# Optimization experiments

Hardware: AMD Instinct MI355X
Metric: run time of the kernel (lower is better)

The kernel has to match this reference:

```python
import jax, jax.numpy as jnp
import numpy as np

N_NODES = 200000
N_EDGES = 6400000
IN_CH, HID, OUT_CH = 14, 16, 2


def gcn_conv(x, W, b, src, dst, n_nodes):
    """GCNConv with self-loops and symmetric normalization (PyG defaults).

    out[i] = sum_{j->i} d[i]^-1/2 d[j]^-1/2 (xW)[j] + d[i]^-1 (xW)[i] + b,
    where d = degree(A + I) computed on the target index.
    """
    h = x @ W  # [N, F_out]
    ones = jnp.ones((src.shape[0],), dtype=x.dtype)
    deg = jax.ops.segment_sum(ones, dst, num_segments=n_nodes) + 1.0  # +1 self-loop
    dinv = jax.lax.rsqrt(deg)  # [N]
    norm = dinv[src] * dinv[dst]  # [E]
    msg = h[src] * norm[:, None]  # [E, F_out] -- dominant memory traffic
    agg = jax.ops.segment_sum(msg, dst, num_segments=n_nodes)
    self_loop = h * (dinv * dinv)[:, None]
    return agg + self_loop + b


def setup_inputs() -> dict:
    key = jax.random.key(0)
    k1, k2, k3, k4, k5 = jax.random.split(key, 5)
    x = jax.random.normal(k1, (N_NODES, IN_CH), dtype=jnp.float32)
    edge_index = jax.random.randint(k2, (2, N_EDGES), 0, N_NODES, dtype=jnp.int64)
    edge_attr = jax.random.normal(k3, (N_EDGES, 1), dtype=jnp.float32)  # unused by GCNConv
    s = 1.0 / np.sqrt(IN_CH)
    W1 = jax.random.uniform(k4, (IN_CH, HID), jnp.float32, -s, s)
    b1 = jnp.zeros((HID,), jnp.float32)
    s2 = 1.0 / np.sqrt(HID)
    W2 = jax.random.uniform(k5, (HID, OUT_CH), jnp.float32, -s2, s2)
    b2 = jnp.zeros((OUT_CH,), jnp.float32)
    return {"x": x, "edge_index": edge_index, "edge_attr": edge_attr,
            "W1": W1, "b1": b1, "W2": W2, "b2": b2}


def reference(x, edge_index, edge_attr, W1, b1, W2, b2):
    src, dst = edge_index[0], edge_index[1]
    n = x.shape[0]
    h = jax.nn.relu(gcn_conv(x, W1, b1, src, dst, n))
    # F.dropout(training=self.training) is identity in eval mode
    out = gcn_conv(h, W2, b2, src, dst, n)
    return out
```

## Files before the change

kernel.cpp:

```cpp
#include <hip/hip_runtime.h>
#include <hip/hip_fp16.h>


constexpr int NN = 200000;
constexpr int NE = 6400000;
constexpr int IC = 14;
constexpr int HC = 16;
constexpr int OC = 2;

constexpr int NBK = 392;
constexpr int NSUB = 8;
constexpr int SCAP = 2816;
constexpr int NSEG = NSUB * NBK;
constexpr int CCAP = NSUB * SCAP;
constexpr int SPT = (SCAP + 1023) / 1024;
constexpr int TILE = 5120;
constexpr int BTH = 512;
constexpr int IPT = TILE / BTH;
constexpr int IPT2 = IPT / 2;
constexpr int NTILE = NE / TILE;
constexpr int OVFCAP = 65536;
constexpr int NM = NN / 32;
constexpr int GSTR = 16;

typedef unsigned long long ull;
typedef float f4v __attribute__((ext_vector_type(4)));

__device__ __forceinline__ int phase_of(unsigned src) {
    return src >= 100000u ? (src >= 150000u ? 3 : 2) : (src >= 50000u ? 1 : 0);
}

__device__ __forceinline__ int xcc_id() {
    int x;
    asm volatile("s_getreg_b32 %0, hwreg(HW_REG_XCC_ID)" : "=s"(x));
    return x & 7;
}

__global__ void k_init(int* __restrict__ gcur, const void* __restrict__ ei,
                       int* __restrict__ flag) {
    int i = blockIdx.x * blockDim.x + threadIdx.x;
    if (i < NSEG) gcur[i * GSTR] = i * SCAP;
    else if (i <= NSEG + 4) gcur[i * GSTR] = 0;
    if (i == 500) {
        const ull* p = (const ull*)ei;
        ull acc = 0ULL;
        for (int k = 0; k < 64; ++k) acc |= (p[k] >> 32);
        *flag = (acc == 0ULL) ? 1 : 0;
    }
}

__global__ __launch_bounds__(BTH, 6) void k_binA(const void* __restrict__ ei,
                                                 const int* __restrict__ flag,
                                                 int* __restrict__ gcur,
                                                 unsigned* __restrict__ binned,
                                                 ull* __restrict__ ovf) {
    __shared__ int hist[NBK];
    __shared__ int lofs[NBK];
    __shared__ int gofs[NBK];
    __shared__ int wsum[BTH / 64];
    __shared__ unsigned stage[TILE];

    int t = threadIdx.x;
    int fl = *flag;
    int tile0 = blockIdx.x * TILE;
    int segbase = xcc_id() * NBK;

    if (t < NBK) hist[t] = 0;
    __syncthreads();

    int dbuf[IPT], sbuf[IPT];
    const int* pw = (const int*)ei;
    if (fl) {
#pragma unroll
        for (int k = 0; k < IPT2; ++k) {
            int e = tile0 + k * (2 * BTH) + 2 * t;
            dbuf[2 * k] = pw[2 * (NE + e)];
            dbuf[2 * k + 1] = pw[2 * (NE + e) + 2];
            sbuf[2 * k] = pw[2 * e];
            sbuf[2 * k + 1] = pw[2 * e + 2];
        }
    } else {
#pragma unroll
        for (int k = 0; k < IPT2; ++k) {
            int e = tile0 + k * (2 * BTH) + 2 * t;
            uint2 dd = *(const uint2*)(pw + NE + e);
            uint2 ss = *(const uint2*)(pw + e);
            dbuf[2 * k] = (int)dd.x;
            dbuf[2 * k + 1] = (int)dd.y;
            sbuf[2 * k] = (int)ss.x;
            sbuf[2 * k + 1] = (int)ss.y;
        }
    }

    unsigned pk[IPT];
    unsigned ra[IPT];
#pragma unroll
    for (int k = 0; k < IPT; ++k) {
        int d = dbuf[k];
        int b = d >> 9;
        int r = atomicAdd(&hist[b], 1);
        pk[k] = ((unsigned)(d & 511) << 18) | (unsigned)sbuf[k];
        ra[k] = ((unsigned)r << 9) | (unsigned)b;
    }
    __syncthreads();

    int h0 = 0, h1 = 0, p = 0;
    if (t < NBK / 2) {
        h0 = hist[2 * t];
        h1 = hist[2 * t + 1];
        p = h0 + h1;
    }
    int lane = t & 63;
    int w = t >> 6;
    int incl = p;
#pragma unroll
    for (int off = 1; off < 64; off <<= 1) {
        int v = __shfl_up(incl, off, 64);
        if (lane >= off) incl += v;
    }
    if (lane == 63) wsum[w] = incl;
    __syncthreads();
    int wbase = 0;
#pragma unroll
    for (int ww = 0; ww < BTH / 64; ++ww) wbase += (ww < w) ? wsum[ww] : 0;
    int ex = wbase + incl - p;
    if (t < NBK / 2) {
        lofs[2 * t] = ex;
        lofs[2 * t + 1] = ex + h0;
    }
    if (t < NBK) gofs[t] = atomicAdd(&gcur[(segbase + t) * GSTR], hist[t]);
    __syncthreads();

#pragma unroll
    for (int k = 0; k < IPT; ++k) {
        int b = (int)(ra[k] & 511u);
        int r = (int)(ra[k] >> 9);
        stage[lofs[b] + r] = pk[k];
    }
    __syncthreads();

    for (int i = t; i < TILE; i += BTH) {
        int b = (i * 313) >> 12;
        if (b > NBK - 1) b = NBK - 1;
        while (b < NBK - 1 && lofs[b + 1] <= i) ++b;
        while (lofs[b] > i) --b;
        unsigned pack = stage[i];
        int seg = segbase + b;
        int dest = gofs[b] + (i - lofs[b]);
        if (dest < (seg + 1) * SCAP) {
            binned[dest] = pack;
        } else {
            int op = atomicAdd(&gcur[NSEG * GSTR], 1);
            if (op < OVFCAP) {
                int d = (b << 9) | (int)(pack >> 18);
                int s = (int)(pack & 0x3FFFF);
                ovf[op] = ((ull)d << 32) | (unsigned)s;
            }
        }
    }
}

__global__ __launch_bounds__(1024, 4) void k_sort(const int* __restrict__ gcur,
                                                  const unsigned* __restrict__ binned,
                                                  const ull* __restrict__ ovf,
                                                  unsigned* __restrict__ csr,
                                                  float* __restrict__ dinv,
                                                  int* __restrict__ rsg,
                                                  unsigned* __restrict__ spl) {
    __shared__ int cnt[2048];
    __shared__ int excl[2048];
    __shared__ int wsum[16];
    __shared__ int nseg[NSUB];
    __shared__ unsigned stage[CCAP];
    int b = blockIdx.x;
    int t = threadIdx.x;
    cnt[t] = 0;
    cnt[t + 1024] = 0;
    if (t < NSUB) {
        int seg = t * NBK + b;
        nseg[t] = min(gcur[seg * GSTR] - seg * SCAP, SCAP);
    }
    __syncthreads();
    int nov = min(gcur[NSEG * GSTR], OVFCAP);

    unsigned srcv[NSUB * SPT];
    unsigned rkv[NSUB * SPT];
#pragma unroll
    for (int s = 0; s < NSUB; ++s) {
        int n = nseg[s];
        int sb = (s * NBK + b) * SCAP;
#pragma unroll
        for (int k = 0; k < SPT; ++k) {
            int i = k * 1024 + t;
            rkv[s * SPT + k] = 0xFFFFFFFFu;
            if (i < n) {
                unsigned pack = binned[sb + i];
                unsigned src = pack & 0x3FFFFu;
                int key = ((int)(pack >> 18) << 2) | phase_of(src);
                int r = atomicAdd(&cnt[key], 1);
                srcv[s * SPT + k] = src;
                rkv[s * SPT + k] = ((unsigned)r << 11) | (unsigned)key;
            }
        }
    }
    __syncthreads();

    int h0 = cnt[2 * t];
    int h1 = cnt[2 * t + 1];
    int p = h0 + h1;
    int lane = t & 63;
    int w = t >> 6;
    int incl = p;
#pragma unroll
    for (int off = 1; off < 64; off <<= 1) {
        int v = __shfl_up(incl, off, 64);
        if (lane >= off) incl += v;
    }
    if (lane == 63) wsum[w] = incl;
    __syncthreads();
    int wbase = 0;
#pragma unroll
    for (int ww = 0; ww < 16; ++ww) wbase += (ww < w) ? wsum[ww] : 0;
    int ex = wbase + incl - p;
    excl[2 * t] = ex;
    excl[2 * t + 1] = ex + h0;
    __syncthreads();

#pragma unroll
    for (int c = 0; c < NSUB * SPT; ++c) {
        unsigned rk = rkv[c];
        if (rk != 0xFFFFFFFFu) {
            int key = (int)(rk & 0x7FFu);
            int r = (int)(rk >> 11);
            stage[excl[key] + r] = srcv[c];
        }
    }

    if (t < 512) {
        int g = (b << 9) + t;
        if (g < NN) {
            int c0 = cnt[4 * t];
            int c1 = cnt[4 * t + 1];
            int c2 = cnt[4 * t + 2];
            int c3 = cnt[4 * t + 3];
            int extra = 0;
            for (int k = 0; k < nov; ++k) extra += ((int)(ovf[k] >> 32) == g);
            dinv[g] = rsqrtf((float)(c0 + c1 + c2 + c3 + extra) + 1.0f);
            rsg[g] = b * CCAP + excl[4 * t];
            spl[g] = (unsigned)c0 | ((unsigned)c1 << 8) |
                     ((unsigned)c2 << 16) | ((unsigned)c3 << 24);
        }
    }
    __syncthreads();

    int total = excl[2047] + cnt[2047];
    int tot4 = (total + 3) >> 2;
    const uint4* st4 = (const uint4*)stage;
    uint4* csr4 = (uint4*)(csr + (size_t)b * CCAP);
#pragma unroll
    for (int k = 0; k < (CCAP / 4 + 1023) / 1024; ++k) {
        int i4 = k * 1024 + t;
        if (i4 < tot4) csr4[i4] = st4[i4];
    }
}

__global__ void k_prep(const float* __restrict__ x, const float* __restrict__ dinv,
                       __half* __restrict__ xph) {
    int i = blockIdx.x * blockDim.x + threadIdx.x;
    if (i >= NN * 16) return;
    int node = i >> 4;
    int c = i & 15;
    float v = (c < IC) ? dinv[node] * x[node * IC + c] : 0.0f;
    xph[i] = __float2half(v);
}

__global__ __launch_bounds__(256) void k_agg1(const int* __restrict__ rsg,
                                              const unsigned* __restrict__ spl,
                                              const unsigned* __restrict__ csr,
                                              const __half* __restrict__ xph,
                                              float* __restrict__ partial) {
    int t = threadIdx.x;
    int q2 = blockIdx.x & 1;
    int blk = blockIdx.x >> 1;
    int g = t >> 3;
    int qq = t & 3;
    int eh = (t >> 2) & 1;
    int i = blk * 32 + g;
    unsigned sp = spl[i];
    int c0 = (int)(sp & 255u);
    int c1 = (int)((sp >> 8) & 255u);
    int beg = rsg[i] + (q2 ? c0 : 0);
    int end = beg + (q2 ? c1 : c0);

    float ax = 0.0f, ay = 0.0f, az = 0.0f, aw = 0.0f;
    int j = beg + eh;
    int s0 = (j < end) ? (int)csr[j] : -1;
    int s1 = (j + 2 < end) ? (int)csr[j + 2] : -1;
    while (j < end) {
        int jn = j + 4;
        int n0 = (jn < end) ? (int)csr[jn] : -1;
        int n1 = (jn + 2 < end) ? (int)csr[jn + 2] : -1;
        uint2 u0 = *(const uint2*)(xph + (size_t)s0 * 16 + 4 * qq);
        float2 f0 = __half22float2(*(__half2*)&u0.x);
        float2 f1 = __half22float2(*(__half2*)&u0.y);
        ax += f0.x;
        ay += f0.y;
        az += f1.x;
        aw += f1.y;
        if (s1 >= 0) {
            uint2 u1 = *(const uint2*)(xph + (size_t)s1 * 16 + 4 * qq);
            float2 f2 = __half22float2(*(__half2*)&u1.x);
            float2 f3 = __half22float2(*(__half2*)&u1.y);
            ax += f2.x;
            ay += f2.y;
            az += f3.x;
            aw += f3.y;
        }
        s0 = n0;
        s1 = n1;
        j = jn;
    }
    ax += __shfl_xor(ax, 4);
    ay += __shfl_xor(ay, 4);
    az += __shfl_xor(az, 4);
    aw += __shfl_xor(aw, 4);
    if (eh == 0) {
        f4v r = {ax, ay, az, aw};
        __builtin_nontemporal_store(
            r, (f4v*)(partial + ((size_t)q2 * NN + i) * 16 + 4 * qq));
    }
}

__global__ __launch_bounds__(256) void k_agg1m(const int* __restrict__ rsg,
                                               const unsigned* __restrict__ spl,
                                               const unsigned* __restrict__ csr,
                                               const __half* __restrict__ xph,
                                               const float* __restrict__ partial,
                                               const int* __restrict__ gcur,
                                               const ull* __restrict__ ovf,
                                               const float* __restrict__ dinv,
                                               const float* __restrict__ W1,
                                               const float* __restrict__ b1,
                                               const float* __restrict__ W2,
                                               const float* __restrict__ b2,
                                               float2* __restrict__ h2bp,
                                               float2* __restrict__ selfout) {
    __shared__ float sW1[IC * HC];
    __shared__ float sb1[HC];
    __shared__ float sW2[HC * OC];
    __shared__ float sb2[OC];
    __shared__ float sAgg[32][17];
    int t = threadIdx.x;
    if (t < IC * HC) sW1[t] = W1[t];
    if (t < HC) sb1[t] = b1[t];
    if (t < HC * OC) sW2[t] = W2[t];
    if (t < OC) sb2[t] = b2[t];

    int g = t >> 3;
    int qq = t & 3;
    int eh = (t >> 2) & 1;
    int i = blockIdx.x * 32 + g;
    unsigned sp = spl[i];
    int c0 = (int)(sp & 255u);
    int c1 = (int)((sp >> 8) & 255u);
    int c2 = (int)((sp >> 16) & 255u);
    int c3 = (int)(sp >> 24);
    int beg = rsg[i] + c0 + c1;
    int end = beg + c2 + c3;

    float ax = 0.0f, ay = 0.0f, az = 0.0f, aw = 0.0f;
    int j = beg + eh;
    int s0 = (j < end) ? (int)csr[j] : -1;
    int s1 = (j + 2 < end) ? (int)csr[j + 2] : -1;
    while (j < end) {
        int jn = j + 4;
        int n0 = (jn < end) ? (int)csr[jn] : -1;
        int n1 = (jn + 2 < end) ? (int)csr[jn + 2] : -1;
        uint2 u0 = *(const uint2*)(xph + (size_t)s0 * 16 + 4 * qq);
        float2 f0 = __half22float2(*(__half2*)&u0.x);
        float2 f1 = __half22float2(*(__half2*)&u0.y);
        ax += f0.x;
        ay += f0.y;
        az += f1.x;
        aw += f1.y;
        if (s1 >= 0) {
            uint2 u1 = *(const uint2*)(xph + (size_t)s1 * 16 + 4 * qq);
            float2 f2 = __half22float2(*(__half2*)&u1.x);
            float2 f3 = __half22float2(*(__half2*)&u1.y);
            ax += f2.x;
            ay += f2.y;
            az += f3.x;
            aw += f3.y;
        }
        s0 = n0;
        s1 = n1;
        j = jn;
    }

    if (eh == 0) {
        f4v a0 = __builtin_nontemporal_load(
            (const f4v*)(partial + (size_t)i * 16 + 4 * qq));
        uint2 us = *(const uint2*)(xph + (size_t)i * 16 + 4 * qq);
        float2 sx = __half22float2(*(__half2*)&us.x);
        float2 sy = __half22float2(*(__half2*)&us.y);
        ax += a0.x + sx.x;
        ay += a0.y + sx.y;
        az += a0.z + sy.x;
        aw += a0.w + sy.y;
    } else {
        f4v a1 = __builtin_nontemporal_load(
            (const f4v*)(partial + ((size_t)NN + i) * 16 + 4 * qq));
        ax += a1.x;
        ay += a1.y;
        az += a1.z;
        aw += a1.w;
    }
    ax += __shfl_xor(ax, 4);
    ay += __shfl_xor(ay, 4);
    az += __shfl_xor(az, 4);
    aw += __shfl_xor(aw, 4);

    float dv = dinv[i];
    if (eh == 0) {
        int nov = min(gcur[NSEG * GSTR], OVFCAP);
        for (int k = 0; k < nov; ++k) {
            ull e = ovf[k];
            if ((int)(e >> 32) == i) {
                int s = (int)(e & 0xFFFFFFFFu);
                int ch = 4 * qq;
                ax += __half2float(xph[(size_t)s * 16 + ch]);
                ay += __half2float(xph[(size_t)s * 16 + ch + 1]);
                az += __half2float(xph[(size_t)s * 16 + ch + 2]);
                aw += __half2float(xph[(size_t)s * 16 + ch + 3]);
            }
        }
        sAgg[g][4 * qq + 0] = dv * ax;
        sAgg[g][4 * qq + 1] = dv * ay;
        sAgg[g][4 * qq + 2] = dv * az;
        sAgg[g][4 * qq + 3] = dv * aw;
    }
    __syncthreads();

    int l8 = t & 7;
    float o0 = 0.0f, o1 = 0.0f;
#pragma unroll
    for (int f2 = 0; f2 < 2; ++f2) {
        int f = 2 * l8 + f2;
        float a = sb1[f];
#pragma unroll
        for (int c = 0; c < IC; ++c) a = fmaf(sAgg[g][c], sW1[c * HC + f], a);
        a = fmaxf(a, 0.0f);
        o0 = fmaf(a, sW2[f * OC + 0], o0);
        o1 = fmaf(a, sW2[f * OC + 1], o1);
    }
    o0 += __shfl_xor(o0, 1);
    o1 += __shfl_xor(o1, 1);
    o0 += __shfl_xor(o0, 2);
    o1 += __shfl_xor(o1, 2);
    o0 += __shfl_xor(o0, 4);
    o1 += __shfl_xor(o1, 4);
    if (l8 == 0) {
        h2bp[i] = make_float2(o0 * dv, o1 * dv);
        selfout[i] = make_float2(o0 * dv * dv + sb2[0], o1 * dv * dv + sb2[1]);
    }
}

__global__ __launch_bounds__(256) void k_agg2(const int* __restrict__ rsg,
                                              const unsigned* __restrict__ spl,
                                              const unsigned* __restrict__ csr,
                                              const int* __restrict__ gcur,
                                              const ull* __restrict__ ovf,
                                              const float* __restrict__ dinv,
                                              const float2* __restrict__ h2bp,
                                              const float2* __restrict__ selfout,
                                              float2* __restrict__ out) {
    int tt = blockIdx.x * 256 + threadIdx.x;
    int i = tt >> 3;
    int h = tt & 7;
    if (i >= NN) return;
    unsigned sp = spl[i];
    int tot = (int)(sp & 255u) + (int)((sp >> 8) & 255u) +
              (int)((sp >> 16) & 255u) + (int)(sp >> 24);
    int beg = rsg[i];
    int end = beg + tot;
    float ax = 0.0f, ay = 0.0f;
    int j = beg + h;
    int s0 = (j < end) ? (int)csr[j] : -1;
    int s1 = (j + 8 < end) ? (int)csr[j + 8] : -1;
    while (j < end) {
        int jn = j + 16;
        int n0 = (jn < end) ? (int)csr[jn] : -1;
        int n1 = (jn + 8 < end) ? (int)csr[jn + 8] : -1;
        float2 h0 = h2bp[s0];
        ax += h0.x;
        ay += h0.y;
        if (s1 >= 0) {
            float2 h1 = h2bp[s1];
            ax += h1.x;
            ay += h1.y;
        }
        s0 = n0;
        s1 = n1;
        j = jn;
    }
    ax += __shfl_xor(ax, 1);
    ay += __shfl_xor(ay, 1);
    ax += __shfl_xor(ax, 2);
    ay += __shfl_xor(ay, 2);
    ax += __shfl_xor(ax, 4);
    ay += __shfl_xor(ay, 4);
    if (h == 0) {
        int nov = min(gcur[NSEG * GSTR], OVFCAP);
        for (int k = 0; k < nov; ++k) {
            ull e = ovf[k];
            if ((int)(e >> 32) == i) {
                float2 hh = h2bp[(int)(e & 0xFFFFFFFFu)];
                ax += hh.x;
                ay += hh.y;
            }
        }
        float dv = dinv[i];
        float2 so = selfout[i];
        out[i] = make_float2(so.x + dv * ax, so.y + dv * ay);
    }
}

extern "C" void kernel_launch(void* const* d_in, const int* in_sizes, int n_in,
                              void* d_out, int out_size, void* d_ws, size_t ws_size,
                              hipStream_t stream) {
    const float* x = (const float*)d_in[0];
    const void* ei = d_in[1];
    const float* W1 = (const float*)d_in[3];
    const float* b1 = (const float*)d_in[4];
    const float* W2 = (const float*)d_in[5];
    const float* b2 = (const float*)d_in[6];
    float* out = (float*)d_out;

    ull* ovf = (ull*)d_ws;
    int* gcur = (int*)(ovf + OVFCAP);
    int* flag = gcur + (NSEG + 5) * GSTR;
    int* rsg = flag + 4;
    unsigned* spl = (unsigned*)(rsg + NN);
    float* dinv = (float*)(spl + NN);
    __half* xph = (__half*)(dinv + NN);
    float2* h2bp = (float2*)(xph + (size_t)NN * 16);
    float2* selfout = h2bp + NN;
    unsigned* binned = (unsigned*)(selfout + NN);
    float* partial = (float*)binned;
    unsigned* csr = binned + (size_t)NSEG * SCAP;

    k_init<<<(NSEG + 5 + 255) / 256, 256, 0, stream>>>(gcur, ei, flag);
    k_binA<<<NTILE, BTH, 0, stream>>>(ei, flag, gcur, binned, ovf);
    k_sort<<<NBK, 1024, 0, stream>>>(gcur, binned, ovf, csr, dinv, rsg, spl);
    k_prep<<<(NN * 16 + 255) / 256, 256, 0, stream>>>(x, dinv, xph);
    k_agg1<<<2 * NM, 256, 0, stream>>>(rsg, spl, csr, xph, partial);
    k_agg1m<<<NM, 256, 0, stream>>>(rsg, spl, csr, xph, partial, gcur, ovf, dinv,
                                    W1, b1, W2, b2, h2bp, selfout);
    k_agg2<<<(NN * 8 + 255) / 256, 256, 0, stream>>>(rsg, spl, csr, gcur, ovf, dinv,
                                                     h2bp, selfout, (float2*)out);
}
```

Before: 285.0 us.

## Fuse feature prescale into sort kernel and widen gather loads to 16 bytes

Removes the separate k_prep launch by having k_sort compute the dinv-scaled half-precision features for its 512 nodes, using dinv kept in shared memory. The layer-1 aggregation kernels change their lane mapping so each lane loads 8 halfs (uint4) per neighbor instead of 4, with four edge-interleaved lanes per channel half reduced by two shuffle stages. This cuts one launch and one pass over dinv and x, and halves the number of gather instructions per edge. In exchange, each thread holds more accumulator registers and k_sort does slightly more work at its end.

```diff
diff --git a/kernel.cpp b/kernel.cpp
--- a/kernel.cpp
+++ b/kernel.cpp
@@ -34,6 +34,15 @@
     int x;
     asm volatile("s_getreg_b32 %0, hwreg(HW_REG_XCC_ID)" : "=s"(x));
     return x & 7;
+}
+
+__device__ __forceinline__ void acc8(float* av, uint4 u) {
+    float2 f0 = __half22float2(*(__half2*)&u.x);
+    float2 f1 = __half22float2(*(__half2*)&u.y);
+    float2 f2 = __half22float2(*(__half2*)&u.z);
+    float2 f3 = __half22float2(*(__half2*)&u.w);
+    av[0] += f0.x; av[1] += f0.y; av[2] += f1.x; av[3] += f1.y;
+    av[4] += f2.x; av[5] += f2.y; av[6] += f3.x; av[7] += f3.y;
 }
 
 __global__ void k_init(int* __restrict__ gcur, const void* __restrict__ ei,
@@ -163,14 +172,17 @@
 __global__ __launch_bounds__(1024, 4) void k_sort(const int* __restrict__ gcur,
                                                   const unsigned* __restrict__ binned,
                                                   const ull* __restrict__ ovf,
+                                                  const float* __restrict__ x,
                                                   unsigned* __restrict__ csr,
                                                   float* __restrict__ dinv,
                                                   int* __restrict__ rsg,
-                                                  unsigned* __restrict__ spl) {
+                                                  unsigned* __restrict__ spl,
+                                                  __half* __restrict__ xph) {
     __shared__ int cnt[2048];
     __shared__ int excl[2048];
     __shared__ int wsum[16];
     __shared__ int nseg[NSUB];
+    __shared__ float sdv[512];
     __shared__ unsigned stage[CCAP];
     int b = blockIdx.x;
     int t = threadIdx.x;
@@ -245,7 +257,9 @@
             int c3 = cnt[4 * t + 3];
             int extra = 0;
             for (int k = 0; k < nov; ++k) extra += ((int)(ovf[k] >> 32) == g);
-            dinv[g] = rsqrtf((float)(c0 + c1 + c2 + c3 + extra) + 1.0f);
+            float dv = rsqrtf((float)(c0 + c1 + c2 + c3 + extra) + 1.0f);
+            dinv[g] = dv;
+            sdv[t] = dv;
             rsg[g] = b * CCAP + excl[4 * t];
             spl[g] = (unsigned)c0 | ((unsigned)c1 << 8) |
                      ((unsigned)c2 << 16) | ((unsigned)c3 << 24);
@@ -262,16 +276,39 @@
         int i4 = k * 1024 + t;
         if (i4 < tot4) csr4[i4] = st4[i4];
     }
-}
-
-__global__ void k_prep(const float* __restrict__ x, const float* __restrict__ dinv,
-                       __half* __restrict__ xph) {
-    int i = blockIdx.x * blockDim.x + threadIdx.x;
-    if (i >= NN * 16) return;
-    int node = i >> 4;
-    int c = i & 15;
-    float v = (c < IC) ? dinv[node] * x[node * IC + c] : 0.0f;
-    xph[i] = __float2half(v);
+
+    {
+        int n512 = t >> 1;
+        int g = (b << 9) + n512;
+        if (g < NN) {
+            float dv = sdv[n512];
+            int cb = 8 * (t & 1);
+            const float* xr = x + (size_t)g * IC;
+            float v[8];
+#pragma unroll
+            for (int c = 0; c < 8; c += 2) {
+                int ch = cb + c;
+                if (ch + 1 < IC) {
+                    float2 xx = *(const float2*)(xr + ch);
+                    v[c] = dv * xx.x;
+                    v[c + 1] = dv * xx.y;
+                } else {
+                    v[c] = 0.0f;
+                    v[c + 1] = 0.0f;
+                }
+            }
+            __half2 p0 = __floats2half2_rn(v[0], v[1]);
+            __half2 p1 = __floats2half2_rn(v[2], v[3]);
+            __half2 p2 = __floats2half2_rn(v[4], v[5]);
+            __half2 p3 = __floats2half2_rn(v[6], v[7]);
+            uint4 pk4;
+            pk4.x = *(unsigned*)&p0;
+            pk4.y = *(unsigned*)&p1;
+            pk4.z = *(unsigned*)&p2;
+            pk4.w = *(unsigned*)&p3;
+            *(uint4*)(xph + (size_t)g * 16 + cb) = pk4;
+        }
+    }
 }
 
 __global__ __launch_bounds__(256) void k_agg1(const int* __restrict__ rsg,
@@ -283,8 +320,9 @@
     int q2 = blockIdx.x & 1;
     int blk = blockIdx.x >> 1;
     int g = t >> 3;
-    int qq = t & 3;
-    int eh = (t >> 2) & 1;
+    int h = t & 7;
+    int qc = h & 1;
+    int eh = h >> 1;
     int i = blk * 32 + g;
     unsigned sp = spl[i];
     int c0 = (int)(sp & 255u);
@@ -292,42 +330,36 @@
     int beg = rsg[i] + (q2 ? c0 : 0);
     int end = beg + (q2 ? c1 : c0);
 
-    float ax = 0.0f, ay = 0.0f, az = 0.0f, aw = 0.0f;
+    float av[8];
+#pragma unroll
+    for (int c = 0; c < 8; ++c) av[c] = 0.0f;
     int j = beg + eh;
     int s0 = (j < end) ? (int)csr[j] : -1;
-    int s1 = (j + 2 < end) ? (int)csr[j + 2] : -1;
+    int s1 = (j + 4 < end) ? (int)csr[j + 4] : -1;
     while (j < end) {
-        int jn = j + 4;
+        int jn = j + 8;
         int n0 = (jn < end) ? (int)csr[jn] : -1;
-        int n1 = (jn + 2 < end) ? (int)csr[jn + 2] : -1;
-        uint2 u0 = *(const uint2*)(xph + (size_t)s0 * 16 + 4 * qq);
-        float2 f0 = __half22float2(*(__half2*)&u0.x);
-        float2 f1 = __half22float2(*(__half2*)&u0.y);
-        ax += f0.x;
-        ay += f0.y;
-        az += f1.x;
-        aw += f1.y;
+        int n1 = (jn + 4 < end) ? (int)csr[jn + 4] : -1;
+        uint4 u0 = *(const uint4*)(xph + (size_t)s0 * 16 + 8 * qc);
+        acc8(av, u0);
         if (s1 >= 0) {
-            uint2 u1 = *(const uint2*)(xph + (size_t)s1 * 16 + 4 * qq);
-            float2 f2 = __half22float2(*(__half2*)&u1.x);
-            float2 f3 = __half22float2(*(__half2*)&u1.y);
-            ax += f2.x;
-            ay += f2.y;
-            az += f3.x;
-            aw += f3.y;
+            uint4 u1 = *(const uint4*)(xph + (size_t)s1 * 16 + 8 * qc);
+            acc8(av, u1);
         }
         s0 = n0;
         s1 = n1;
         j = jn;
     }
-    ax += __shfl_xor(ax, 4);
-    ay += __shfl_xor(ay, 4);
-    az += __shfl_xor(az, 4);
-    aw += __shfl_xor(aw, 4);
+#pragma unroll
+    for (int c = 0; c < 8; ++c) av[c] += __shfl_xor(av[c], 2);
+#pragma unroll
+    for (int c = 0; c < 8; ++c) av[c] += __shfl_xor(av[c], 4);
     if (eh == 0) {
-        f4v r = {ax, ay, az, aw};
-        __builtin_nontemporal_store(
-            r, (f4v*)(partial + ((size_t)q2 * NN + i) * 16 + 4 * qq));
+        f4v r0 = {av[0], av[1], av[2], av[3]};
+        f4v r1 = {av[4], av[5], av[6], av[7]};
+        float* dst = partial + ((size_t)q2 * NN + i) * 16 + 8 * qc;
+        __builtin_nontemporal_store(r0, (f4v*)dst);
+        __builtin_nontemporal_store(r1, (f4v*)(dst + 4));
     }
 }
 
@@ -357,8 +389,9 @@
     if (t < OC) sb2[t] = b2[t];
 
     int g = t >> 3;
-    int qq = t & 3;
-    int eh = (t >> 2) & 1;
+    int h = t & 7;
+    int qc = h & 1;
+    int eh = h >> 1;
     int i = blockIdx.x * 32 + g;
     unsigned sp = spl[i];
     int c0 = (int)(sp & 255u);
@@ -368,29 +401,21 @@
     int beg = rsg[i] + c0 + c1;
     int end = beg + c2 + c3;
 
-    float ax = 0.0f, ay = 0.0f, az = 0.0f, aw = 0.0f;
+    float av[8];
+#pragma unroll
+    for (int c = 0; c < 8; ++c) av[c] = 0.0f;
     int j = beg + eh;
     int s0 = (j < end) ? (int)csr[j] : -1;
-    int s1 = (j + 2 < end) ? (int)csr[j + 2] : -1;
+    int s1 = (j + 4 < end) ? (int)csr[j + 4] : -1;
     while (j < end) {
-        int jn = j + 4;
+        int jn = j + 8;
         int n0 = (jn < end) ? (int)csr[jn] : -1;
-        int n1 = (jn + 2 < end) ? (int)csr[jn + 2] : -1;
-        uint2 u0 = *(const uint2*)(xph + (size_t)s0 * 16 + 4 * qq);
-        float2 f0 = __half22float2(*(__half2*)&u0.x);
-        float2 f1 = __half22float2(*(__half2*)&u0.y);
-        ax += f0.x;
-        ay += f0.y;
-        az += f1.x;
-        aw += f1.y;
+        int n1 = (jn + 4 < end) ? (int)csr[jn + 4] : -1;
+        uint4 u0 = *(const uint4*)(xph + (size_t)s0 * 16 + 8 * qc);
+        acc8(av, u0);
         if (s1 >= 0) {
-            uint2 u1 = *(const uint2*)(xph + (size_t)s1 * 16 + 4 * qq);
-            float2 f2 = __half22float2(*(__half2*)&u1.x);
-            float2 f3 = __half22float2(*(__half2*)&u1.y);
-            ax += f2.x;
-            ay += f2.y;
-            az += f3.x;
-            aw += f3.y;
+            uint4 u1 = *(const uint4*)(xph + (size_t)s1 * 16 + 8 * qc);
+            acc8(av, u1);
         }
         s0 = n0;
         s1 = n1;
@@ -398,27 +423,24 @@
     }
 
     if (eh == 0) {
-        f4v a0 = __builtin_nontemporal_load(
-            (const f4v*)(partial + (size_t)i * 16 + 4 * qq));
-        uint2 us = *(const uint2*)(xph + (size_t)i * 16 + 4 * qq);
-        float2 sx = __half22float2(*(__half2*)&us.x);
-        float2 sy = __half22float2(*(__half2*)&us.y);
-        ax += a0.x + sx.x;
-        ay += a0.y + sx.y;
-        az += a0.z + sy.x;
-        aw += a0.w + sy.y;
-    } else {
-        f4v a1 = __builtin_nontemporal_load(
-            (const f4v*)(partial + ((size_t)NN + i) * 16 + 4 * qq));
-        ax += a1.x;
-        ay += a1.y;
-        az += a1.z;
-        aw += a1.w;
-    }
-    ax += __shfl_xor(ax, 4);
-    ay += __shfl_xor(ay, 4);
-    az += __shfl_xor(az, 4);
-    aw += __shfl_xor(aw, 4);
+        const float* ps = partial + (size_t)i * 16 + 8 * qc;
+        f4v p0 = __builtin_nontemporal_load((const f4v*)ps);
+        f4v p1 = __builtin_nontemporal_load((const f4v*)(ps + 4));
+        uint4 us = *(const uint4*)(xph + (size_t)i * 16 + 8 * qc);
+        acc8(av, us);
+        av[0] += p0.x; av[1] += p0.y; av[2] += p0.z; av[3] += p0.w;
+        av[4] += p1.x; av[5] += p1.y; av[6] += p1.z; av[7] += p1.w;
+    } else if (eh == 1) {
+        const float* ps = partial + ((size_t)NN + i) * 16 + 8 * qc;
+        f4v p0 = __builtin_nontemporal_load((const f4v*)ps);
+        f4v p1 = __builtin_nontemporal_load((const f4v*)(ps + 4));
+        av[0] += p0.x; av[1] += p0.y; av[2] += p0.z; av[3] += p0.w;
+        av[4] += p1.x; av[5] += p1.y; av[6] += p1.z; av[7] += p1.w;
+    }
+#pragma unroll
+    for (int c = 0; c < 8; ++c) av[c] += __shfl_xor(av[c], 2);
+#pragma unroll
+    for (int c = 0; c < 8; ++c) av[c] += __shfl_xor(av[c], 4);
 
     float dv = dinv[i];
     if (eh == 0) {
@@ -427,17 +449,13 @@
             ull e = ovf[k];
             if ((int)(e >> 32) == i) {
                 int s = (int)(e & 0xFFFFFFFFu);
-                int ch = 4 * qq;
-                ax += __half2float(xph[(size_t)s * 16 + ch]);
-                ay += __half2float(xph[(size_t)s * 16 + ch + 1]);
-                az += __half2float(xph[(size_t)s * 16 + ch + 2]);
-                aw += __half2float(xph[(size_t)s * 16 + ch + 3]);
+#pragma unroll
+                for (int c = 0; c < 8; ++c)
+                    av[c] += __half2float(xph[(size_t)s * 16 + 8 * qc + c]);
             }
         }
-        sAgg[g][4 * qq + 0] = dv * ax;
-        sAgg[g][4 * qq + 1] = dv * ay;
-        sAgg[g][4 * qq + 2] = dv * az;
-        sAgg[g][4 * qq + 3] = dv * aw;
+#pragma unroll
+        for (int c = 0; c < 8; ++c) sAgg[g][8 * qc + c] = dv * av[c];
     }
     __syncthreads();
 
@@ -551,8 +569,7 @@
 
     k_init<<<(NSEG + 5 + 255) / 256, 256, 0, stream>>>(gcur, ei, flag);
     k_binA<<<NTILE, BTH, 0, stream>>>(ei, flag, gcur, binned, ovf);
-    k_sort<<<NBK, 1024, 0, stream>>>(gcur, binned, ovf, csr, dinv, rsg, spl);
-    k_prep<<<(NN * 16 + 255) / 256, 256, 0, stream>>>(x, dinv, xph);
+    k_sort<<<NBK, 1024, 0, stream>>>(gcur, binned, ovf, x, csr, dinv, rsg, spl, xph);
     k_agg1<<<2 * NM, 256, 0, stream>>>(rsg, spl, csr, xph, partial);
     k_agg1m<<<NM, 256, 0, stream>>>(rsg, spl, csr, xph, partial, gcur, ovf, dinv,
                                     W1, b1, W2, b2, h2bp, selfout);
```

New measurement: 271.6 us. 4.7% less time.
